# Performance work log

Measured on AMD Instinct MI355X. Metric: run time of the kernel, lower is better.

## Reference

```python
import math
import jax, jax.numpy as jnp
import numpy as np

B, T, E, H = 1, 2048, 2048, 16
D = E // H // 2  # head_dim = 64
DEPTH = 12
LAMBDA_INIT = 0.8 - 0.6 * math.exp(-0.3 * DEPTH)
EPS = 1e-5
NEG = -1e30


def rotary_cos_sin(seqlen, dim):
    # matches flash-attn RotaryEmbedding: inv_freq over even indices, base 10000
    inv_freq = 1.0 / (10000.0 ** (jnp.arange(0, dim, 2, dtype=jnp.float32) / dim))
    t = jnp.arange(seqlen, dtype=jnp.float32)
    freqs = jnp.outer(t, inv_freq)  # [T, D/2]
    return jnp.cos(freqs), jnp.sin(freqs)


def apply_rotary_interleaved(x, cos, sin):
    # x: [B, T, nH, D]; rotate interleaved pairs (x0,x1),(x2,x3),...
    x1 = x[..., 0::2]
    x2 = x[..., 1::2]
    c = cos[None, :, None, :]
    s = sin[None, :, None, :]
    o1 = x1 * c - x2 * s
    o2 = x1 * s + x2 * c
    return jnp.stack([o1, o2], axis=-1).reshape(x.shape)


def causal_attn_pair(q, k, v1, v2, mask, scale):
    # q,k,v*: [B, T, H, D]; shared softmax over (q,k), applied to both v1 and v2
    s = jnp.einsum('bthd,bshd->bhts', q, k) * scale
    s = jnp.where(mask, s, NEG)
    a = jax.nn.softmax(s, axis=-1)
    o1 = jnp.einsum('bhts,bshd->bthd', a, v1)
    o2 = jnp.einsum('bhts,bshd->bthd', a, v2)
    return jnp.concatenate([o1, o2], axis=-1)  # [B, T, H, 2D]


def setup_inputs() -> dict:
    key = jax.random.key(0)
    ks = jax.random.split(key, 10)
    return {
        'query': jax.random.normal(ks[0], (B, T, E), dtype=jnp.float32),
        'Wq': jax.random.normal(ks[1], (E, E), dtype=jnp.float32) * 0.02,
        'Wk': jax.random.normal(ks[2], (E, E), dtype=jnp.float32) * 0.02,
        'Wv': jax.random.normal(ks[3], (E, E), dtype=jnp.float32) * 0.02,
        'Wout': jax.random.normal(ks[4], (E, E), dtype=jnp.float32) * 0.02,
        'lambda_q1': jax.random.normal(ks[5], (D,), dtype=jnp.float32) * 0.1,
        'lambda_k1': jax.random.normal(ks[6], (D,), dtype=jnp.float32) * 0.1,
        'lambda_q2': jax.random.normal(ks[7], (D,), dtype=jnp.float32) * 0.1,
        'lambda_k2': jax.random.normal(ks[8], (D,), dtype=jnp.float32) * 0.1,
        'rms_weight': jnp.ones((2 * D,), dtype=jnp.float32),
    }


def reference(query, Wq, Wk, Wv, Wout, lambda_q1, lambda_k1, lambda_q2, lambda_k2, rms_weight):
    bsz, tgt_len, embed_dim = query.shape
    cos, sin = rotary_cos_sin(tgt_len, D)
    scale = D ** (-0.5)
    mask = jnp.tril(jnp.ones((tgt_len, tgt_len), dtype=bool))[None, None]

    q = (query @ Wq).reshape(bsz, tgt_len, 2 * H, D)
    k = (query @ Wk).reshape(bsz, tgt_len, 2 * H, D)
    v = (query @ Wv).reshape(bsz, tgt_len, H, 2, D)

    q = apply_rotary_emb = apply_rotary_interleaved(q, cos, sin)
    k = apply_rotary_interleaved(k, cos, sin)

    q = q.reshape(bsz, tgt_len, H, 2, D)
    k = k.reshape(bsz, tgt_len, H, 2, D)
    q1, q2 = q[:, :, :, 0], q[:, :, :, 1]
    k1, k2 = k[:, :, :, 0], k[:, :, :, 1]
    v1, v2 = v[:, :, :, 0], v[:, :, :, 1]

    attn1 = causal_attn_pair(q1, k1, v1, v2, mask, scale)  # [B,T,H,2D]
    attn2 = causal_attn_pair(q2, k2, v1, v2, mask, scale)

    lambda_1 = jnp.exp(jnp.sum(lambda_q1 * lambda_k1))
    lambda_2 = jnp.exp(jnp.sum(lambda_q2 * lambda_k2))
    lambda_full = lambda_1 - lambda_2 + LAMBDA_INIT

    f1 = jnp.fft.rfft(attn1, axis=1)
    f2 = jnp.fft.rfft(attn2, axis=1)
    attn_freq = f1 - lambda_full * f2

    n_freq = attn_freq.shape[1]
    sigma = 0.3 / 2.0  # cutoff_ratio / 2, gaussian window
    x = jnp.linspace(0.0, 1.0, n_freq)
    filt = jnp.exp(-0.5 * (x / sigma) ** 2)
    attn_freq = attn_freq * filt[None, :, None, None]

    attn = jnp.fft.irfft(attn_freq, n=tgt_len, axis=1)  # [B,T,H,2D]

    # RMSNorm over last dim (2*head_dim) with affine weight
    attn = attn * jax.lax.rsqrt(jnp.mean(attn * attn, axis=-1, keepdims=True) + EPS) * rms_weight
    attn = attn * (1.0 - LAMBDA_INIT)

    attn = attn.reshape(bsz, tgt_len, H * 2 * D)
    return attn @ Wout
```

## Files before the change

### kernel.cpp

```cpp
#include <hip/hip_runtime.h>
#include <math.h>

#define LAMBDA_INIT_F 0.7836057665316245f
#define ONE_MINUS_LI  0.2163942334683755f

typedef unsigned short ushort_t;
typedef unsigned int   uint32;
typedef unsigned long long u64;
typedef __attribute__((ext_vector_type(8))) short short8;
typedef __attribute__((ext_vector_type(4))) float f32x4;

__device__ __forceinline__ ushort_t f2bf(float f) {
    union { float f; uint32 u; } x; x.f = f;
    uint32 r = (x.u + 0x7fffu + ((x.u >> 16) & 1u)) >> 16;
    return (ushort_t)r;
}

__device__ __forceinline__ void gld16(ushort_t* lds, const ushort_t* g) {
    __builtin_amdgcn_global_load_lds(
        (const __attribute__((address_space(1))) uint32*)g,
        (__attribute__((address_space(3))) uint32*)lds,
        16, 0, 0);
}

__global__ __launch_bounds__(64) void lambda_kernel(
    const float* __restrict__ lq1, const float* __restrict__ lk1,
    const float* __restrict__ lq2, const float* __restrict__ lk2,
    float* __restrict__ lam)
{
    int l = threadIdx.x;
    float p1 = lq1[l] * lk1[l];
    float p2 = lq2[l] * lk2[l];
    for (int off = 32; off; off >>= 1) {
        p1 += __shfl_down(p1, off);
        p2 += __shfl_down(p2, off);
    }
    if (l == 0) lam[0] = expf(p1) - expf(p2) + LAMBDA_INIT_F;
}

__global__ __launch_bounds__(256) void gfilt_kernel(float* __restrict__ g)
{
    __shared__ float red[4];
    const int j = blockIdx.x;
    int tau = j - 64;
    int ta = tau < 0 ? -tau : tau;
    const int tid = threadIdx.x;
    float acc = 0.0f;
    for (int k = tid; k <= 1024; k += 256) {
        float w = (k == 0 || k == 1024) ? 1.0f : 2.0f;
        float r = (float)k * (1.0f / 153.6f);
        float f = expf(-0.5f * r * r);
        int m = (k * ta) & 2047;
        float ang = (float)m * 3.0679615757712823e-3f;
        acc += w * f * cosf(ang);
    }
    for (int off = 32; off; off >>= 1) acc += __shfl_down(acc, off);
    if ((tid & 63) == 0) red[tid >> 6] = acc;
    __syncthreads();
    if (tid == 0)
        g[j] = (red[0] + red[1] + red[2] + red[3]) * (1.0f / 2048.0f);
}

__global__ __launch_bounds__(256) void rottab(float* __restrict__ ct, float* __restrict__ st)
{
    int id = blockIdx.x * 256 + threadIdx.x;
    int t = id >> 5, i = id & 31;
    double inv = exp(-0.28782313662425575 * (double)i);
    double a = (double)t * inv;
    ct[id] = (float)cos(a);
    st[id] = (float)sin(a);
}

__global__ __launch_bounds__(256) void cvt_bf16(const float* __restrict__ s, ushort_t* __restrict__ d)
{
    int i = (blockIdx.x * 256 + threadIdx.x) * 8;
    float4 a = *(const float4*)(s + i);
    float4 b = *(const float4*)(s + i + 4);
    uint4 pk;
    pk.x = (uint32)f2bf(a.x) | ((uint32)f2bf(a.y) << 16);
    pk.y = (uint32)f2bf(a.z) | ((uint32)f2bf(a.w) << 16);
    pk.z = (uint32)f2bf(b.x) | ((uint32)f2bf(b.y) << 16);
    pk.w = (uint32)f2bf(b.z) | ((uint32)f2bf(b.w) << 16);
    *(uint4*)(d + i) = pk;
}

__global__ __launch_bounds__(256) void wtrans(
    const float* __restrict__ Wq, const float* __restrict__ Wk,
    const float* __restrict__ Wv, const float* __restrict__ Wo,
    ushort_t* __restrict__ Tq, ushort_t* __restrict__ Tk,
    ushort_t* __restrict__ Tv, ushort_t* __restrict__ To)
{
    int z = blockIdx.z;
    const float* S = (z == 0) ? Wq : (z == 1) ? Wk : (z == 2) ? Wv : Wo;
    ushort_t* Dt = (z == 0) ? Tq : (z == 1) ? Tk : (z == 2) ? Tv : To;
    bool perm = (z < 2);
    __shared__ float Ls[64 * 65];
    const int tid = threadIdx.x;
    const int n0 = blockIdx.x * 64, k0 = blockIdx.y * 64;
    #pragma unroll
    for (int it = 0; it < 4; ++it) {
        int kk = it * 16 + (tid >> 4);
        int nn = (tid & 15) * 4;
        float4 v = *(const float4*)(S + (size_t)(k0 + kk) * 2048 + n0 + nn);
        Ls[(nn + 0) * 65 + kk] = v.x;
        Ls[(nn + 1) * 65 + kk] = v.y;
        Ls[(nn + 2) * 65 + kk] = v.z;
        Ls[(nn + 3) * 65 + kk] = v.w;
    }
    __syncthreads();
    int nl = tid >> 2, kc = (tid & 3) * 16;
    int ng = n0 + nl;
    int nd = perm ? ((ng & ~63) | ((ng & 1) << 5) | ((ng & 63) >> 1)) : ng;
    uint4 p0, p1;
    const float* row = Ls + nl * 65 + kc;
    p0.x = (uint32)f2bf(row[0])  | ((uint32)f2bf(row[1])  << 16);
    p0.y = (uint32)f2bf(row[2])  | ((uint32)f2bf(row[3])  << 16);
    p0.z = (uint32)f2bf(row[4])  | ((uint32)f2bf(row[5])  << 16);
    p0.w = (uint32)f2bf(row[6])  | ((uint32)f2bf(row[7])  << 16);
    p1.x = (uint32)f2bf(row[8])  | ((uint32)f2bf(row[9])  << 16);
    p1.y = (uint32)f2bf(row[10]) | ((uint32)f2bf(row[11]) << 16);
    p1.z = (uint32)f2bf(row[12]) | ((uint32)f2bf(row[13]) << 16);
    p1.w = (uint32)f2bf(row[14]) | ((uint32)f2bf(row[15]) << 16);
    *(uint4*)(Dt + (size_t)nd * 2048 + k0 + kc) = p0;
    *(uint4*)(Dt + (size_t)nd * 2048 + k0 + kc + 8) = p1;
}

__global__ __launch_bounds__(256) void gemm_qkv(
    const ushort_t* __restrict__ A, const ushort_t* __restrict__ WT,
    ushort_t* __restrict__ q1, ushort_t* __restrict__ q2,
    ushort_t* __restrict__ k1, ushort_t* __restrict__ k2,
    ushort_t* __restrict__ v1T, ushort_t* __restrict__ v2T,
    const float* __restrict__ ctab, const float* __restrict__ stab)
{
    __shared__ ushort_t As[8192];
    __shared__ ushort_t Bs[8192];
    const int tid = threadIdx.x;
    const int w = tid >> 6, lane = tid & 63;
    const int quad = lane >> 4, l15 = lane & 15;
    const int wr = w >> 1, wc = w & 1;
    const int rb = blockIdx.y * 128, cb = blockIdx.x * 128;

    f32x4 acc[4][4];
    #pragma unroll
    for (int i = 0; i < 4; ++i)
        #pragma unroll
        for (int j = 0; j < 4; ++j) acc[i][j] = (f32x4)0.0f;

    for (int k0 = 0; k0 < 2048; k0 += 64) {
        #pragma unroll
        for (int u = 0; u < 4; ++u) {
            int off = (w * 4 + u) * 512;
            int Lc = (off >> 3) + lane;
            int row = Lc >> 3, cc = (Lc & 7) ^ (row & 7);
            gld16(As + off, A + (size_t)(rb + row) * 2048 + k0 + cc * 8);
            gld16(Bs + off, WT + (size_t)(cb + row) * 2048 + k0 + cc * 8);
        }
        __syncthreads();
        #pragma unroll
        for (int ks = 0; ks < 2; ++ks) {
            short8 af[4], bfr[4];
            #pragma unroll
            for (int mi = 0; mi < 4; ++mi) {
                int r = wr * 64 + mi * 16 + l15;
                af[mi] = *(const short8*)(As + r * 64 + ((ks * 4 + quad) ^ (r & 7)) * 8);
            }
            #pragma unroll
            for (int nj = 0; nj < 4; ++nj) {
                int r = wc * 64 + nj * 16 + l15;
                bfr[nj] = *(const short8*)(Bs + r * 64 + ((ks * 4 + quad) ^ (r & 7)) * 8);
            }
            #pragma unroll
            for (int mi = 0; mi < 4; ++mi)
                #pragma unroll
                for (int nj = 0; nj < 4; ++nj)
                    acc[mi][nj] = __builtin_amdgcn_mfma_f32_16x16x32_bf16(
                        af[mi], bfr[nj], acc[mi][nj], 0, 0, 0);
        }
        __syncthreads();
    }

    const int region = cb >> 11;
    const int nloc = cb & 2047;
    if (region < 2) {
        int head2 = (nloc + wc * 64) >> 6;
        ushort_t* b1 = region ? k1 : q1;
        ushort_t* b2 = region ? k2 : q2;
        ushort_t* dst = ((head2 & 1) ? b2 : b1) + (size_t)(head2 >> 1) * 2048 * 64;
        #pragma unroll
        for (int mi = 0; mi < 4; ++mi)
            #pragma unroll
            for (int r = 0; r < 4; ++r) {
                int t = rb + wr * 64 + mi * 16 + quad * 4 + r;
                const float* ctr = ctab + t * 32;
                const float* str = stab + t * 32;
                #pragma unroll
                for (int nj = 0; nj < 2; ++nj) {
                    int i = nj * 16 + l15;
                    float c = ctr[i], s = str[i];
                    float x1 = acc[mi][nj][r], x2 = acc[mi][nj + 2][r];
                    dst[(size_t)t * 64 + i]      = f2bf(x1 * c - x2 * s);
                    dst[(size_t)t * 64 + 32 + i] = f2bf(x1 * s + x2 * c);
                }
            }
    } else {
        #pragma unroll
        for (int mi = 0; mi < 4; ++mi)
            #pragma unroll
            for (int nj = 0; nj < 4; ++nj) {
                int cg = nloc + wc * 64 + nj * 16 + l15;
                int hh = cg >> 7, pr = (cg >> 6) & 1, d = cg & 63;
                int tb = rb + wr * 64 + mi * 16 + quad * 4;
                ushort_t* dst = (pr ? v2T : v1T) + ((size_t)(hh * 64 + d)) * 2048 + tb;
                u64 pk = (u64)f2bf(acc[mi][nj][0])
                       | ((u64)f2bf(acc[mi][nj][1]) << 16)
                       | ((u64)f2bf(acc[mi][nj][2]) << 32)
                       | ((u64)f2bf(acc[mi][nj][3]) << 48);
                *(u64*)dst = pk;
            }
    }
}

#define PSTRIDE 88

__device__ __forceinline__ void attn_step(
    const ushort_t* __restrict__ Kb, const ushort_t* __restrict__ V1b,
    const ushort_t* __restrict__ V2b, ushort_t* __restrict__ pw,
    const short8* qb, f32x4* O, float& m_i, float& l_i,
    int quad, int l15, int row_l, bool diag)
{
    f32x4 s[4];
    #pragma unroll
    for (int j = 0; j < 4; ++j) s[j] = (f32x4)0.0f;
    #pragma unroll
    for (int ks = 0; ks < 2; ++ks)
        #pragma unroll
        for (int j = 0; j < 4; ++j) {
            int r = j * 16 + l15;
            short8 kf = *(const short8*)(Kb + r * 64 + ((ks * 4 + quad) ^ (r & 7)) * 8);
            s[j] = __builtin_amdgcn_mfma_f32_16x16x32_bf16(kf, qb[ks], s[j], 0, 0, 0);
        }
    float pv[16];
    float mx = -1e30f;
    #pragma unroll
    for (int j = 0; j < 4; ++j)
        #pragma unroll
        for (int r = 0; r < 4; ++r) {
            float v = s[j][r] * 0.125f;
            if (diag) {
                int kp = j * 16 + quad * 4 + r;
                v = (kp <= row_l) ? v : -1e30f;
            }
            pv[j * 4 + r] = v;
            mx = fmaxf(mx, v);
        }
    mx = fmaxf(mx, __shfl_xor(mx, 16));
    mx = fmaxf(mx, __shfl_xor(mx, 32));
    float newm = fmaxf(m_i, mx);
    float alpha = __expf(m_i - newm);
    float sum = 0.0f;
    ushort_t pb[16];
    #pragma unroll
    for (int i = 0; i < 16; ++i) {
        float p = __expf(pv[i] - newm);
        sum += p;
        pb[i] = f2bf(p);
    }
    sum += __shfl_xor(sum, 16);
    sum += __shfl_xor(sum, 32);
    l_i = l_i * alpha + sum;
    m_i = newm;
    #pragma unroll
    for (int j = 0; j < 4; ++j) {
        u64 pk = (u64)pb[j * 4] | ((u64)pb[j * 4 + 1] << 16)
               | ((u64)pb[j * 4 + 2] << 32) | ((u64)pb[j * 4 + 3] << 48);
        *(u64*)(pw + l15 * PSTRIDE + j * 16 + quad * 4) = pk;
    }
    float av0 = __shfl(alpha, quad * 4 + 0);
    float av1 = __shfl(alpha, quad * 4 + 1);
    float av2 = __shfl(alpha, quad * 4 + 2);
    float av3 = __shfl(alpha, quad * 4 + 3);
    #pragma unroll
    for (int nt = 0; nt < 8; ++nt) {
        O[nt][0] *= av0; O[nt][1] *= av1; O[nt][2] *= av2; O[nt][3] *= av3;
    }
    #pragma unroll
    for (int ks = 0; ks < 2; ++ks) {
        short8 pf = *(const short8*)(pw + l15 * PSTRIDE + ks * 32 + quad * 8);
        #pragma unroll
        for (int nt = 0; nt < 8; ++nt) {
            const ushort_t* Vs = (nt < 4) ? V1b : V2b;
            int d = (nt & 3) * 16 + l15;
            short8 vf = *(const short8*)(Vs + d * 64 + ((ks * 4 + quad) ^ (d & 7)) * 8);
            O[nt] = __builtin_amdgcn_mfma_f32_16x16x32_bf16(pf, vf, O[nt], 0, 0, 0);
        }
    }
}

__global__ __launch_bounds__(256) void attn_pipe(
    const ushort_t* __restrict__ q1, const ushort_t* __restrict__ k1,
    const ushort_t* __restrict__ q2, const ushort_t* __restrict__ k2,
    const ushort_t* __restrict__ v1T, const ushort_t* __restrict__ v2T,
    float* __restrict__ X, const float* __restrict__ lam_ptr)
{
    __shared__ ushort_t Tt[4][4096];
    __shared__ ushort_t Ps[4][2][16 * PSTRIDE];

    const int tid = threadIdx.x;
    const int w = tid >> 6, lane = tid & 63;
    const int quad = lane >> 4, l15 = lane & 15;
    const int b = blockIdx.x;
    const int h = b & 15;
    const int qt = 31 - (b >> 4);
    const float lam = lam_ptr[0];
    const int row_l = w * 16 + l15;

    const ushort_t* k1h = k1 + (size_t)h * 2048 * 64;
    const ushort_t* k2h = k2 + (size_t)h * 2048 * 64;
    const ushort_t* v1h = v1T + (size_t)h * 64 * 2048;
    const ushort_t* v2h = v2T + (size_t)h * 64 * 2048;

    short8 qb1[2], qb2[2];
    {
        const ushort_t* q1p = q1 + ((size_t)h * 2048 + qt * 64 + w * 16 + l15) * 64 + quad * 8;
        const ushort_t* q2p = q2 + ((size_t)h * 2048 + qt * 64 + w * 16 + l15) * 64 + quad * 8;
        qb1[0] = *(const short8*)(q1p);      qb1[1] = *(const short8*)(q1p + 32);
        qb2[0] = *(const short8*)(q2p);      qb2[1] = *(const short8*)(q2p + 32);
    }

    int ci[2], koff[2], voff[2];
    #pragma unroll
    for (int u = 0; u < 2; ++u) {
        ci[u] = tid * 2 + u;
        int row = ci[u] >> 3, cc = (ci[u] & 7) ^ (row & 7);
        koff[u] = row * 64 + cc * 8;
        voff[u] = row * 2048 + cc * 8;
    }

    short8 sK1[2], sK2[2], sV1[2], sV2[2];

    #pragma unroll
    for (int u = 0; u < 2; ++u) {
        sK1[u] = *(const short8*)(k1h + koff[u]);
        sK2[u] = *(const short8*)(k2h + koff[u]);
        sV1[u] = *(const short8*)(v1h + voff[u]);
        sV2[u] = *(const short8*)(v2h + voff[u]);
    }
    #pragma unroll
    for (int u = 0; u < 2; ++u) {
        *(short8*)(&Tt[0][ci[u] * 8]) = sK1[u];
        *(short8*)(&Tt[1][ci[u] * 8]) = sK2[u];
        *(short8*)(&Tt[2][ci[u] * 8]) = sV1[u];
        *(short8*)(&Tt[3][ci[u] * 8]) = sV2[u];
    }
    __syncthreads();

    f32x4 O1[8], O2[8];
    #pragma unroll
    for (int i = 0; i < 8; ++i) { O1[i] = (f32x4)0.0f; O2[i] = (f32x4)0.0f; }
    float m1 = -1e30f, l1 = 0.0f, m2 = -1e30f, l2 = 0.0f;

    for (int kt = 0; kt <= qt; ++kt) {
        if (kt < qt) {
            int kb = (kt + 1) * 4096, vb = (kt + 1) * 64;
            #pragma unroll
            for (int u = 0; u < 2; ++u) {
                sK1[u] = *(const short8*)(k1h + kb + koff[u]);
                sK2[u] = *(const short8*)(k2h + kb + koff[u]);
                sV1[u] = *(const short8*)(v1h + vb + voff[u]);
                sV2[u] = *(const short8*)(v2h + vb + voff[u]);
            }
        }
        const bool diag = (kt == qt);
        attn_step(Tt[0], Tt[2], Tt[3], &Ps[w][0][0], qb1, O1, m1, l1, quad, l15, row_l, diag);
        attn_step(Tt[1], Tt[2], Tt[3], &Ps[w][1][0], qb2, O2, m2, l2, quad, l15, row_l, diag);
        __syncthreads();
        if (kt < qt) {
            #pragma unroll
            for (int u = 0; u < 2; ++u) {
                *(short8*)(&Tt[0][ci[u] * 8]) = sK1[u];
                *(short8*)(&Tt[1][ci[u] * 8]) = sK2[u];
                *(short8*)(&Tt[2][ci[u] * 8]) = sV1[u];
                *(short8*)(&Tt[3][ci[u] * 8]) = sV2[u];
            }
            __syncthreads();
        }
    }

    float r10 = 1.0f / __shfl(l1, quad * 4 + 0);
    float r11 = 1.0f / __shfl(l1, quad * 4 + 1);
    float r12 = 1.0f / __shfl(l1, quad * 4 + 2);
    float r13 = 1.0f / __shfl(l1, quad * 4 + 3);
    float r20 = lam / __shfl(l2, quad * 4 + 0);
    float r21 = lam / __shfl(l2, quad * 4 + 1);
    float r22 = lam / __shfl(l2, quad * 4 + 2);
    float r23 = lam / __shfl(l2, quad * 4 + 3);
    int tb = qt * 64 + w * 16 + quad * 4;
    #pragma unroll
    for (int nt = 0; nt < 8; ++nt) {
        int col = h * 128 + nt * 16 + l15;
        X[(size_t)(tb + 0) * 2048 + col] = O1[nt][0] * r10 - O2[nt][0] * r20;
        X[(size_t)(tb + 1) * 2048 + col] = O1[nt][1] * r11 - O2[nt][1] * r21;
        X[(size_t)(tb + 2) * 2048 + col] = O1[nt][2] * r12 - O2[nt][2] * r22;
        X[(size_t)(tb + 3) * 2048 + col] = O1[nt][3] * r13 - O2[nt][3] * r23;
    }
}

__global__ __launch_bounds__(256) void conv_t(
    const float* __restrict__ X, const float* __restrict__ g, float* __restrict__ Y)
{
    __shared__ float Xs[192 * 64];
    __shared__ float gs[129];
    const int tid = threadIdx.x;
    const int c0 = blockIdx.x * 64, t0 = blockIdx.y * 64;
    const int c = tid & 63, tg = tid >> 6;
    for (int j = tg; j < 192; j += 4)
        Xs[j * 64 + c] = X[(size_t)((t0 - 64 + j) & 2047) * 2048 + c0 + c];
    if (tid < 129) gs[tid] = g[tid];
    __syncthreads();
    float accv[16];
    #pragma unroll
    for (int i = 0; i < 16; ++i) accv[i] = 0.0f;
    const int tl0 = tg * 16;
    for (int tap = 0; tap < 129; ++tap) {
        float gv = gs[tap];
        int base = (tl0 + 128 - tap) * 64 + c;
        #pragma unroll
        for (int i = 0; i < 16; ++i) accv[i] += gv * Xs[base + i * 64];
    }
    #pragma unroll
    for (int i = 0; i < 16; ++i)
        Y[(size_t)(t0 + tl0 + i) * 2048 + c0 + c] = accv[i];
}

__global__ __launch_bounds__(64) void rms_bf(
    const float* __restrict__ Y, const float* __restrict__ wgt, ushort_t* __restrict__ yb)
{
    int grp = blockIdx.x;
    int t = grp >> 4, hh = grp & 15, l = threadIdx.x;
    size_t base = (size_t)t * 2048 + hh * 128;
    float a = Y[base + l];
    float b = Y[base + 64 + l];
    float ss = a * a + b * b;
    for (int off = 32; off; off >>= 1) ss += __shfl_down(ss, off);
    ss = __shfl(ss, 0);
    float r = rsqrtf(ss * (1.0f / 128.0f) + 1e-5f) * ONE_MINUS_LI;
    yb[base + l]      = f2bf(a * r * wgt[l]);
    yb[base + 64 + l] = f2bf(b * r * wgt[64 + l]);
}

__global__ __launch_bounds__(256) void gemm_out(
    const ushort_t* __restrict__ A, const ushort_t* __restrict__ BT,
    float* __restrict__ C)
{
    __shared__ ushort_t As[4096];
    __shared__ ushort_t Bs[8192];
    const int tid = threadIdx.x;
    const int w = tid >> 6, lane = tid & 63;
    const int quad = lane >> 4, l15 = lane & 15;
    const int wr = w >> 1, wc = w & 1;
    const int rb = blockIdx.y * 64, cb = blockIdx.x * 128;

    f32x4 acc[2][4];
    #pragma unroll
    for (int i = 0; i < 2; ++i)
        #pragma unroll
        for (int j = 0; j < 4; ++j) acc[i][j] = (f32x4)0.0f;

    for (int k0 = 0; k0 < 2048; k0 += 64) {
        #pragma unroll
        for (int u = 0; u < 2; ++u) {
            int off = (w * 2 + u) * 512;
            int Lc = (off >> 3) + lane;
            int row = Lc >> 3, cc = (Lc & 7) ^ (row & 7);
            gld16(As + off, A + (size_t)(rb + row) * 2048 + k0 + cc * 8);
        }
        #pragma unroll
        for (int u = 0; u < 4; ++u) {
            int off = (w * 4 + u) * 512;
            int Lc = (off >> 3) + lane;
            int row = Lc >> 3, cc = (Lc & 7) ^ (row & 7);
            gld16(Bs + off, BT + (size_t)(cb + row) * 2048 + k0 + cc * 8);
        }
        __syncthreads();
        #pragma unroll
        for (int ks = 0; ks < 2; ++ks) {
            short8 af[2], bfr[4];
            #pragma unroll
            for (int mi = 0; mi < 2; ++mi) {
                int r = wr * 32 + mi * 16 + l15;
                af[mi] = *(const short8*)(As + r * 64 + ((ks * 4 + quad) ^ (r & 7)) * 8);
            }
            #pragma unroll
            for (int nj = 0; nj < 4; ++nj) {
                int r = wc * 64 + nj * 16 + l15;
                bfr[nj] = *(const short8*)(Bs + r * 64 + ((ks * 4 + quad) ^ (r & 7)) * 8);
            }
            #pragma unroll
            for (int mi = 0; mi < 2; ++mi)
                #pragma unroll
                for (int nj = 0; nj < 4; ++nj)
                    acc[mi][nj] = __builtin_amdgcn_mfma_f32_16x16x32_bf16(
                        af[mi], bfr[nj], acc[mi][nj], 0, 0, 0);
        }
        __syncthreads();
    }

    #pragma unroll
    for (int mi = 0; mi < 2; ++mi)
        #pragma unroll
        for (int nj = 0; nj < 4; ++nj) {
            int cg = cb + wc * 64 + nj * 16 + l15;
            #pragma unroll
            for (int r = 0; r < 4; ++r) {
                int t = rb + wr * 32 + mi * 16 + quad * 4 + r;
                C[(size_t)t * 2048 + cg] = acc[mi][nj][r];
            }
        }
}

extern "C" void kernel_launch(void* const* d_in, const int* in_sizes, int n_in,
                              void* d_out, int out_size, void* d_ws, size_t ws_size,
                              hipStream_t stream)
{
    const float* query = (const float*)d_in[0];
    const float* Wq    = (const float*)d_in[1];
    const float* Wk    = (const float*)d_in[2];
    const float* Wv    = (const float*)d_in[3];
    const float* Wout  = (const float*)d_in[4];
    const float* lq1   = (const float*)d_in[5];
    const float* lk1   = (const float*)d_in[6];
    const float* lq2   = (const float*)d_in[7];
    const float* lk2   = (const float*)d_in[8];
    const float* rmsw  = (const float*)d_in[9];
    float* out = (float*)d_out;

    const size_t MB = 1ull << 20;
    char* W = (char*)d_ws;
    ushort_t* WqT   = (ushort_t*)(W + 0 * MB);
    ushort_t* WkT   = (ushort_t*)(W + 8 * MB);
    ushort_t* WvT   = (ushort_t*)(W + 16 * MB);
    ushort_t* WoutT = (ushort_t*)(W + 24 * MB);
    ushort_t* qb    = (ushort_t*)(W + 32 * MB);
    ushort_t* q1    = (ushort_t*)(W + 40 * MB);
    ushort_t* q2    = (ushort_t*)(W + 44 * MB);
    ushort_t* k1    = (ushort_t*)(W + 48 * MB);
    ushort_t* k2    = (ushort_t*)(W + 52 * MB);
    ushort_t* v1T   = (ushort_t*)(W + 56 * MB);
    ushort_t* v2T   = (ushort_t*)(W + 60 * MB);
    float*    X     = (float*)   (W + 64 * MB);
    float*    Y     = (float*)   (W + 32 * MB);
    ushort_t* ybf   = (ushort_t*)(W + 48 * MB);
    float*    ctab  = (float*)   (W + 80 * MB);
    float*    stab  = (float*)   (W + 80 * MB + 256 * 1024);
    float*    gbuf  = (float*)   (W + 80 * MB + 512 * 1024);
    float*    lam   = (float*)   (W + 80 * MB + 520 * 1024);

    lambda_kernel<<<1, 64, 0, stream>>>(lq1, lk1, lq2, lk2, lam);
    gfilt_kernel<<<129, 256, 0, stream>>>(gbuf);
    rottab<<<256, 256, 0, stream>>>(ctab, stab);
    cvt_bf16<<<2048, 256, 0, stream>>>(query, qb);
    wtrans<<<dim3(32, 32, 4), 256, 0, stream>>>(Wq, Wk, Wv, Wout, WqT, WkT, WvT, WoutT);

    gemm_qkv<<<dim3(48, 16), 256, 0, stream>>>(qb, WqT, q1, q2, k1, k2, v1T, v2T, ctab, stab);

    attn_pipe<<<512, 256, 0, stream>>>(q1, k1, q2, k2, v1T, v2T, X, lam);

    conv_t<<<dim3(32, 32), 256, 0, stream>>>(X, gbuf, Y);
    rms_bf<<<32768, 64, 0, stream>>>(Y, rmsw, ybf);

    gemm_out<<<dim3(16, 32), 256, 0, stream>>>(ybf, WoutT, out);
}
```

Baseline: 366.2 us.

## Fuse setup kernels, fold softmax scale into Q, and run conv+RMS as MFMA

Three small setup kernels are merged into one launch. The softmax scale and log2(e) factor are folded into Q at projection time, so attention uses exp2 and packs probabilities to bf16 by truncation instead of rounding. The attention output is written transposed in bf16. The scalar fp32 time-convolution plus separate RMSNorm kernel are replaced by one fused kernel that runs the convolution as a bf16 MFMA against a banded Toeplitz matrix, with PSTRIDE and launch bounds also adjusted. This cuts launches and intermediate fp32 traffic, at the cost of lower precision in the conv input and in the softmax probabilities.

```diff
diff --git a/kernel.cpp b/kernel.cpp
--- a/kernel.cpp
+++ b/kernel.cpp
@@ -3,6 +3,7 @@
 
 #define LAMBDA_INIT_F 0.7836057665316245f
 #define ONE_MINUS_LI  0.2163942334683755f
+#define QSCL          0.18033688011112042f
 
 typedef unsigned short ushort_t;
 typedef unsigned int   uint32;
@@ -23,52 +24,60 @@
         16, 0, 0);
 }
 
-__global__ __launch_bounds__(64) void lambda_kernel(
+__global__ __launch_bounds__(256) void setup_kernel(
     const float* __restrict__ lq1, const float* __restrict__ lk1,
     const float* __restrict__ lq2, const float* __restrict__ lk2,
-    float* __restrict__ lam)
-{
-    int l = threadIdx.x;
-    float p1 = lq1[l] * lk1[l];
-    float p2 = lq2[l] * lk2[l];
-    for (int off = 32; off; off >>= 1) {
-        p1 += __shfl_down(p1, off);
-        p2 += __shfl_down(p2, off);
-    }
-    if (l == 0) lam[0] = expf(p1) - expf(p2) + LAMBDA_INIT_F;
-}
-
-__global__ __launch_bounds__(256) void gfilt_kernel(float* __restrict__ g)
+    float* __restrict__ lam, float* __restrict__ g,
+    float* __restrict__ ct, float* __restrict__ st)
 {
     __shared__ float red[4];
-    const int j = blockIdx.x;
-    int tau = j - 64;
-    int ta = tau < 0 ? -tau : tau;
+    const int b = blockIdx.x;
     const int tid = threadIdx.x;
-    float acc = 0.0f;
-    for (int k = tid; k <= 1024; k += 256) {
-        float w = (k == 0 || k == 1024) ? 1.0f : 2.0f;
-        float r = (float)k * (1.0f / 153.6f);
-        float f = expf(-0.5f * r * r);
-        int m = (k * ta) & 2047;
-        float ang = (float)m * 3.0679615757712823e-3f;
-        acc += w * f * cosf(ang);
-    }
-    for (int off = 32; off; off >>= 1) acc += __shfl_down(acc, off);
-    if ((tid & 63) == 0) red[tid >> 6] = acc;
-    __syncthreads();
-    if (tid == 0)
-        g[j] = (red[0] + red[1] + red[2] + red[3]) * (1.0f / 2048.0f);
-}
-
-__global__ __launch_bounds__(256) void rottab(float* __restrict__ ct, float* __restrict__ st)
-{
-    int id = blockIdx.x * 256 + threadIdx.x;
-    int t = id >> 5, i = id & 31;
-    double inv = exp(-0.28782313662425575 * (double)i);
-    double a = (double)t * inv;
-    ct[id] = (float)cos(a);
-    st[id] = (float)sin(a);
+    if (b == 0) {
+        if (tid < 64) {
+            float p1 = lq1[tid] * lk1[tid];
+            float p2 = lq2[tid] * lk2[tid];
+            for (int off = 32; off; off >>= 1) {
+                p1 += __shfl_down(p1, off);
+                p2 += __shfl_down(p2, off);
+            }
+            if (tid == 0) lam[0] = expf(p1) - expf(p2) + LAMBDA_INIT_F;
+        }
+    } else if (b <= 129) {
+        const int j = b - 1;
+        int tau = j - 64;
+        int ta = tau < 0 ? -tau : tau;
+        float acc = 0.0f;
+        for (int k = tid; k <= 1024; k += 256) {
+            float w = (k == 0 || k == 1024) ? 1.0f : 2.0f;
+            float r = (float)k * (1.0f / 153.6f);
+            float f = expf(-0.5f * r * r);
+            int m = (k * ta) & 2047;
+            float ang = (float)m * 3.0679615757712823e-3f;
+            acc += w * f * cosf(ang);
+        }
+        for (int off = 32; off; off >>= 1) acc += __shfl_down(acc, off);
+        if ((tid & 63) == 0) red[tid >> 6] = acc;
+        __syncthreads();
+        if (tid == 0)
+            g[j] = (red[0] + red[1] + red[2] + red[3]) * (1.0f / 2048.0f);
+    } else {
+        int id = (b - 130) * 256 + tid;
+        int t = id >> 5, i = id & 31;
+        double inv = exp(-0.28782313662425575 * (double)i);
+        double a = (double)t * inv;
+        ct[id] = (float)cos(a);
+        st[id] = (float)sin(a);
+    }
+}
+
+__global__ __launch_bounds__(192) void gmat_kernel(
+    const float* __restrict__ g, ushort_t* __restrict__ Gm)
+{
+    int i = blockIdx.x, j = threadIdx.x;
+    int idx = i - j + 128;
+    float v = (idx >= 0 && idx <= 128) ? g[idx] : 0.0f;
+    Gm[i * 192 + j] = f2bf(v);
 }
 
 __global__ __launch_bounds__(256) void cvt_bf16(const float* __restrict__ s, ushort_t* __restrict__ d)
@@ -182,6 +191,7 @@
     const int region = cb >> 11;
     const int nloc = cb & 2047;
     if (region < 2) {
+        const float scl = region ? 1.0f : QSCL;
         int head2 = (nloc + wc * 64) >> 6;
         ushort_t* b1 = region ? k1 : q1;
         ushort_t* b2 = region ? k2 : q2;
@@ -198,8 +208,8 @@
                     int i = nj * 16 + l15;
                     float c = ctr[i], s = str[i];
                     float x1 = acc[mi][nj][r], x2 = acc[mi][nj + 2][r];
-                    dst[(size_t)t * 64 + i]      = f2bf(x1 * c - x2 * s);
-                    dst[(size_t)t * 64 + 32 + i] = f2bf(x1 * s + x2 * c);
+                    dst[(size_t)t * 64 + i]      = f2bf((x1 * c - x2 * s) * scl);
+                    dst[(size_t)t * 64 + 32 + i] = f2bf((x1 * s + x2 * c) * scl);
                 }
             }
     } else {
@@ -220,7 +230,7 @@
     }
 }
 
-#define PSTRIDE 88
+#define PSTRIDE 72
 
 __device__ __forceinline__ void attn_step(
     const ushort_t* __restrict__ Kb, const ushort_t* __restrict__ V1b,
@@ -245,7 +255,7 @@
     for (int j = 0; j < 4; ++j)
         #pragma unroll
         for (int r = 0; r < 4; ++r) {
-            float v = s[j][r] * 0.125f;
+            float v = s[j][r];
             if (diag) {
                 int kp = j * 16 + quad * 4 + r;
                 v = (kp <= row_l) ? v : -1e30f;
@@ -256,14 +266,13 @@
     mx = fmaxf(mx, __shfl_xor(mx, 16));
     mx = fmaxf(mx, __shfl_xor(mx, 32));
     float newm = fmaxf(m_i, mx);
-    float alpha = __expf(m_i - newm);
+    float alpha = __builtin_amdgcn_exp2f(m_i - newm);
+    float p[16];
     float sum = 0.0f;
-    ushort_t pb[16];
     #pragma unroll
     for (int i = 0; i < 16; ++i) {
-        float p = __expf(pv[i] - newm);
-        sum += p;
-        pb[i] = f2bf(p);
+        p[i] = __builtin_amdgcn_exp2f(pv[i] - newm);
+        sum += p[i];
     }
     sum += __shfl_xor(sum, 16);
     sum += __shfl_xor(sum, 32);
@@ -271,8 +280,11 @@
     m_i = newm;
     #pragma unroll
     for (int j = 0; j < 4; ++j) {
-        u64 pk = (u64)pb[j * 4] | ((u64)pb[j * 4 + 1] << 16)
-               | ((u64)pb[j * 4 + 2] << 32) | ((u64)pb[j * 4 + 3] << 48);
+        uint32 lo = (__float_as_uint(p[j * 4 + 0]) >> 16)
+                  | (__float_as_uint(p[j * 4 + 1]) & 0xffff0000u);
+        uint32 hi = (__float_as_uint(p[j * 4 + 2]) >> 16)
+                  | (__float_as_uint(p[j * 4 + 3]) & 0xffff0000u);
+        u64 pk = (u64)lo | ((u64)hi << 32);
         *(u64*)(pw + l15 * PSTRIDE + j * 16 + quad * 4) = pk;
     }
     float av0 = __shfl(alpha, quad * 4 + 0);
@@ -296,11 +308,11 @@
     }
 }
 
-__global__ __launch_bounds__(256) void attn_pipe(
+__global__ __launch_bounds__(256, 3) void attn_pipe(
     const ushort_t* __restrict__ q1, const ushort_t* __restrict__ k1,
     const ushort_t* __restrict__ q2, const ushort_t* __restrict__ k2,
     const ushort_t* __restrict__ v1T, const ushort_t* __restrict__ v2T,
-    float* __restrict__ X, const float* __restrict__ lam_ptr)
+    ushort_t* __restrict__ XT, const float* __restrict__ lam_ptr)
 {
     __shared__ ushort_t Tt[4][4096];
     __shared__ ushort_t Ps[4][2][16 * PSTRIDE];
@@ -397,55 +409,90 @@
     int tb = qt * 64 + w * 16 + quad * 4;
     #pragma unroll
     for (int nt = 0; nt < 8; ++nt) {
-        int col = h * 128 + nt * 16 + l15;
-        X[(size_t)(tb + 0) * 2048 + col] = O1[nt][0] * r10 - O2[nt][0] * r20;
-        X[(size_t)(tb + 1) * 2048 + col] = O1[nt][1] * r11 - O2[nt][1] * r21;
-        X[(size_t)(tb + 2) * 2048 + col] = O1[nt][2] * r12 - O2[nt][2] * r22;
-        X[(size_t)(tb + 3) * 2048 + col] = O1[nt][3] * r13 - O2[nt][3] * r23;
-    }
-}
-
-__global__ __launch_bounds__(256) void conv_t(
-    const float* __restrict__ X, const float* __restrict__ g, float* __restrict__ Y)
-{
-    __shared__ float Xs[192 * 64];
-    __shared__ float gs[129];
+        int c = h * 128 + nt * 16 + l15;
+        float v0 = O1[nt][0] * r10 - O2[nt][0] * r20;
+        float v1 = O1[nt][1] * r11 - O2[nt][1] * r21;
+        float v2 = O1[nt][2] * r12 - O2[nt][2] * r22;
+        float v3 = O1[nt][3] * r13 - O2[nt][3] * r23;
+        u64 pk = (u64)f2bf(v0) | ((u64)f2bf(v1) << 16)
+               | ((u64)f2bf(v2) << 32) | ((u64)f2bf(v3) << 48);
+        *(u64*)(XT + (size_t)c * 2048 + tb) = pk;
+    }
+}
+
+__global__ __launch_bounds__(256) void conv_rms(
+    const ushort_t* __restrict__ XT, const ushort_t* __restrict__ Gm,
+    const float* __restrict__ rmsw, ushort_t* __restrict__ yb)
+{
+    __shared__ float ssum[4][64];
     const int tid = threadIdx.x;
-    const int c0 = blockIdx.x * 64, t0 = blockIdx.y * 64;
-    const int c = tid & 63, tg = tid >> 6;
-    for (int j = tg; j < 192; j += 4)
-        Xs[j * 64 + c] = X[(size_t)((t0 - 64 + j) & 2047) * 2048 + c0 + c];
-    if (tid < 129) gs[tid] = g[tid];
+    const int w = tid >> 6, lane = tid & 63;
+    const int quad = lane >> 4, l15 = lane & 15;
+    const int t0 = blockIdx.x * 64;
+    const int h = blockIdx.y;
+
+    f32x4 acc[2][4];
+    #pragma unroll
+    for (int i = 0; i < 2; ++i)
+        #pragma unroll
+        for (int j = 0; j < 4; ++j) acc[i][j] = (f32x4)0.0f;
+
+    #pragma unroll
+    for (int ks = 0; ks < 6; ++ks) {
+        int tbk = (t0 - 64 + ks * 32) & 2047;
+        short8 af[2], bfr[4];
+        #pragma unroll
+        for (int mi = 0; mi < 2; ++mi)
+            af[mi] = *(const short8*)(XT + (size_t)(h * 128 + w * 32 + mi * 16 + l15) * 2048
+                                      + tbk + quad * 8);
+        #pragma unroll
+        for (int nj = 0; nj < 4; ++nj)
+            bfr[nj] = *(const short8*)(Gm + (nj * 16 + l15) * 192 + ks * 32 + quad * 8);
+        #pragma unroll
+        for (int mi = 0; mi < 2; ++mi)
+            #pragma unroll
+            for (int nj = 0; nj < 4; ++nj)
+                acc[mi][nj] = __builtin_amdgcn_mfma_f32_16x16x32_bf16(
+                    af[mi], bfr[nj], acc[mi][nj], 0, 0, 0);
+    }
+
+    float part[4];
+    #pragma unroll
+    for (int nj = 0; nj < 4; ++nj) {
+        float p = 0.0f;
+        #pragma unroll
+        for (int mi = 0; mi < 2; ++mi)
+            #pragma unroll
+            for (int r = 0; r < 4; ++r)
+                p += acc[mi][nj][r] * acc[mi][nj][r];
+        p += __shfl_xor(p, 16);
+        p += __shfl_xor(p, 32);
+        part[nj] = p;
+    }
+    if (quad == 0) {
+        #pragma unroll
+        for (int nj = 0; nj < 4; ++nj) ssum[w][nj * 16 + l15] = part[nj];
+    }
     __syncthreads();
-    float accv[16];
-    #pragma unroll
-    for (int i = 0; i < 16; ++i) accv[i] = 0.0f;
-    const int tl0 = tg * 16;
-    for (int tap = 0; tap < 129; ++tap) {
-        float gv = gs[tap];
-        int base = (tl0 + 128 - tap) * 64 + c;
-        #pragma unroll
-        for (int i = 0; i < 16; ++i) accv[i] += gv * Xs[base + i * 64];
-    }
-    #pragma unroll
-    for (int i = 0; i < 16; ++i)
-        Y[(size_t)(t0 + tl0 + i) * 2048 + c0 + c] = accv[i];
-}
-
-__global__ __launch_bounds__(64) void rms_bf(
-    const float* __restrict__ Y, const float* __restrict__ wgt, ushort_t* __restrict__ yb)
-{
-    int grp = blockIdx.x;
-    int t = grp >> 4, hh = grp & 15, l = threadIdx.x;
-    size_t base = (size_t)t * 2048 + hh * 128;
-    float a = Y[base + l];
-    float b = Y[base + 64 + l];
-    float ss = a * a + b * b;
-    for (int off = 32; off; off >>= 1) ss += __shfl_down(ss, off);
-    ss = __shfl(ss, 0);
-    float r = rsqrtf(ss * (1.0f / 128.0f) + 1e-5f) * ONE_MINUS_LI;
-    yb[base + l]      = f2bf(a * r * wgt[l]);
-    yb[base + 64 + l] = f2bf(b * r * wgt[64 + l]);
+
+    float4 rw0 = *(const float4*)(rmsw + w * 32 + quad * 4);
+    float4 rw1 = *(const float4*)(rmsw + w * 32 + 16 + quad * 4);
+    #pragma unroll
+    for (int nj = 0; nj < 4; ++nj) {
+        int col = nj * 16 + l15;
+        float tot = ssum[0][col] + ssum[1][col] + ssum[2][col] + ssum[3][col];
+        float s = rsqrtf(tot * (1.0f / 128.0f) + 1e-5f) * ONE_MINUS_LI;
+        #pragma unroll
+        for (int mi = 0; mi < 2; ++mi) {
+            float4 rw = mi ? rw1 : rw0;
+            u64 pk = (u64)f2bf(acc[mi][nj][0] * s * rw.x)
+                   | ((u64)f2bf(acc[mi][nj][1] * s * rw.y) << 16)
+                   | ((u64)f2bf(acc[mi][nj][2] * s * rw.z) << 32)
+                   | ((u64)f2bf(acc[mi][nj][3] * s * rw.w) << 48);
+            *(u64*)(yb + (size_t)(t0 + nj * 16 + l15) * 2048
+                    + h * 128 + w * 32 + mi * 16 + quad * 4) = pk;
+        }
+    }
 }
 
 __global__ __launch_bounds__(256) void gemm_out(
@@ -547,26 +594,24 @@
     ushort_t* k2    = (ushort_t*)(W + 52 * MB);
     ushort_t* v1T   = (ushort_t*)(W + 56 * MB);
     ushort_t* v2T   = (ushort_t*)(W + 60 * MB);
-    float*    X     = (float*)   (W + 64 * MB);
-    float*    Y     = (float*)   (W + 32 * MB);
-    ushort_t* ybf   = (ushort_t*)(W + 48 * MB);
+    ushort_t* XT    = (ushort_t*)(W + 64 * MB);
+    ushort_t* ybf   = (ushort_t*)(W + 72 * MB);
     float*    ctab  = (float*)   (W + 80 * MB);
     float*    stab  = (float*)   (W + 80 * MB + 256 * 1024);
     float*    gbuf  = (float*)   (W + 80 * MB + 512 * 1024);
-    float*    lam   = (float*)   (W + 80 * MB + 520 * 1024);
-
-    lambda_kernel<<<1, 64, 0, stream>>>(lq1, lk1, lq2, lk2, lam);
-    gfilt_kernel<<<129, 256, 0, stream>>>(gbuf);
-    rottab<<<256, 256, 0, stream>>>(ctab, stab);
+    float*    lam   = (float*)   (W + 80 * MB + 516 * 1024);
+    ushort_t* Gm    = (ushort_t*)(W + 80 * MB + 520 * 1024);
+
+    setup_kernel<<<386, 256, 0, stream>>>(lq1, lk1, lq2, lk2, lam, gbuf, ctab, stab);
+    gmat_kernel<<<64, 192, 0, stream>>>(gbuf, Gm);
     cvt_bf16<<<2048, 256, 0, stream>>>(query, qb);
     wtrans<<<dim3(32, 32, 4), 256, 0, stream>>>(Wq, Wk, Wv, Wout, WqT, WkT, WvT, WoutT);
 
     gemm_qkv<<<dim3(48, 16), 256, 0, stream>>>(qb, WqT, q1, q2, k1, k2, v1T, v2T, ctab, stab);
 
-    attn_pipe<<<512, 256, 0, stream>>>(q1, k1, q2, k2, v1T, v2T, X, lam);
-
-    conv_t<<<dim3(32, 32), 256, 0, stream>>>(X, gbuf, Y);
-    rms_bf<<<32768, 64, 0, stream>>>(Y, rmsw, ybf);
+    attn_pipe<<<512, 256, 0, stream>>>(q1, k1, q2, k2, v1T, v2T, XT, lam);
+
+    conv_rms<<<dim3(32, 16), 256, 0, stream>>>(XT, Gm, rmsw, ybf);
 
     gemm_out<<<dim3(16, 32), 256, 0, stream>>>(ybf, WoutT, out);
 }
```

After: 431.1 us. 17.7% more time.
